# Optimization experiments

Measured on AMD Instinct MI355X. Metric: run time of the kernel, lower is better.

The kernel has to match this reference:

```python
import jax, jax.numpy as jnp
import numpy as np

N = 131072          # events
N_OBS = 64          # observables
HID = [512, 512, 512]          # trunk hidden widths
SUB_HID = [512, 256]           # per-pair subnetwork hidden widths
P = 3                          # number of pairings


def _glorot(key, shape):
    fan_in, fan_out = shape[-2], shape[-1]
    lim = np.sqrt(6.0 / (fan_in + fan_out)).astype(np.float32)
    return jax.random.uniform(key, shape, jnp.float32, -lim, lim)


def setup_inputs() -> dict:
    key = jax.random.key(0)
    ks = jax.random.split(key, 16)
    x = jax.random.normal(ks[0], (N, N_OBS), jnp.float32)
    y = jax.random.randint(ks[1], (N,), 0, 3)
    pairs = jnp.array([[0, 1], [0, 2], [1, 2]], dtype=jnp.int32)
    # trunk params
    W0 = _glorot(ks[2], (N_OBS, HID[0])); b0 = jnp.zeros((HID[0],), jnp.float32)
    W1 = _glorot(ks[3], (HID[0], HID[1])); b1 = jnp.zeros((HID[1],), jnp.float32)
    W2 = _glorot(ks[4], (HID[1], HID[2])); b2 = jnp.zeros((HID[2],), jnp.float32)
    # stacked per-pair subnetwork params (all P subnets share shapes)
    SW0 = _glorot(ks[5], (P, HID[2], SUB_HID[0])); Sb0 = jnp.zeros((P, SUB_HID[0]), jnp.float32)
    SW1 = _glorot(ks[6], (P, SUB_HID[0], SUB_HID[1])); Sb1 = jnp.zeros((P, SUB_HID[1]), jnp.float32)
    SW2 = _glorot(ks[7], (P, SUB_HID[1], 1)); Sb2 = jnp.zeros((P, 1), jnp.float32)
    return {"x": x, "y": y, "pairs": pairs,
            "W0": W0, "b0": b0, "W1": W1, "b1": b1, "W2": W2, "b2": b2,
            "SW0": SW0, "Sb0": Sb0, "SW1": SW1, "Sb1": Sb1, "SW2": SW2, "Sb2": Sb2}


def reference(x, y, pairs, W0, b0, W1, b1, W2, b2, SW0, Sb0, SW1, Sb1, SW2, Sb2):
    relu = jax.nn.relu
    # Trunk. Note: in the torch module with dropout_prob>0, the first Linear sits at
    # layer index 1, so the activation is applied to the raw input as well (eval-mode
    # dropout == identity). We reproduce that exactly.
    h = relu(x) @ W0 + b0
    h = relu(h) @ W1 + b1
    repr_ = relu(h) @ W2 + b2                      # [N, HID[-1]]

    # Per-pair membership masks (jit-safe stand-in for the variable-size gather):
    # mask[p, n] = True iff y[n] is one of the two labels of pairing p.
    mask = (y[None, :] == pairs[:, 0:1]) | (y[None, :] == pairs[:, 1:2])  # [P, N] bool

    # Per-pair RatioModel subnetworks, batched over the pair dim.
    # Same activation-before-every-Linear pattern as the trunk (dropout indices).
    hs = jnp.einsum('nd,pdh->pnh', relu(repr_), SW0) + Sb0[:, None, :]
    hs = jnp.einsum('pnh,phk->pnk', relu(hs), SW1) + Sb1[:, None, :]
    logit = jnp.einsum('pnk,pko->pno', relu(hs), SW2) + Sb2[:, None, :]  # [P, N, 1]
    s_hat = jnp.clip(jax.nn.sigmoid(logit[..., 0]), 1e-9, None)          # [P, N]
    r_hat = (1.0 - s_hat) / s_hat                                        # [P, N]

    maskf = mask.astype(s_hat.dtype)
    return repr_, r_hat * maskf, s_hat * maskf, mask
```

## Files before the change

### kernel.cpp

```cpp
#include <hip/hip_runtime.h>
#include <stdint.h>

#define NE 131072

typedef __attribute__((ext_vector_type(8))) short bf16x8;
typedef __attribute__((ext_vector_type(4))) float f32x4;

static __device__ __forceinline__ unsigned short f2bf(float f) {
  unsigned u = __float_as_uint(f);
  u += 0x7FFF + ((u >> 16) & 1);
  return (unsigned short)(u >> 16);
}
static __device__ __forceinline__ float bf2f(unsigned short h) {
  return __uint_as_float((unsigned)h << 16);
}
static __device__ __forceinline__ void gload_lds16(const void* g, void* l) {
  __builtin_amdgcn_global_load_lds(
      (const __attribute__((address_space(1))) unsigned*)g,
      (__attribute__((address_space(3))) unsigned*)l, 16, 0, 0);
}

__global__ void weight_prep(const float* __restrict__ W0, const float* __restrict__ W1,
                            const float* __restrict__ W2, const float* __restrict__ SW0,
                            const float* __restrict__ SW1, const float* __restrict__ SW2,
                            unsigned short* W0t, unsigned short* W1t,
                            unsigned short* W2t, unsigned short* SW0t,
                            unsigned short* SW1t, unsigned short* SW2b) {
  __shared__ float tile[32][33];
  const int u = blockIdx.y;
  const float* src; unsigned short* dst; int K, Nc;
  if (u == 0)      { src = W0;  dst = W0t;  K = 64;  Nc = 512; }
  else if (u == 1) { src = W1;  dst = W1t;  K = 512; Nc = 512; }
  else if (u == 2) { src = W2;  dst = W2t;  K = 512; Nc = 512; }
  else if (u < 6)  { int p = u - 3; src = SW0 + (long)p * 512 * 512; dst = SW0t + (long)p * 512 * 512; K = 512; Nc = 512; }
  else if (u < 9)  { int p = u - 6; src = SW1 + (long)p * 512 * 256; dst = SW1t + (long)p * 256 * 512; K = 512; Nc = 256; }
  else             { int p = u - 9; src = SW2 + (long)p * 256;       dst = SW2b + (long)p * 256;       K = 256; Nc = 1; }
  const int tkn = K >> 5;
  const int tk = blockIdx.x % tkn, tn = blockIdx.x / tkn;
  if (tn >= ((Nc + 31) >> 5)) return;
  const int k0 = tk * 32, n0 = tn * 32;
  const int tx = threadIdx.x & 31, ty = threadIdx.x >> 5;
  if (n0 + tx < Nc)
#pragma unroll
    for (int j = 0; j < 4; ++j)
      tile[ty * 4 + j][tx] = src[(long)(k0 + ty * 4 + j) * Nc + n0 + tx];
  __syncthreads();
#pragma unroll
  for (int j = 0; j < 4; ++j) {
    int n = n0 + ty * 4 + j;
    if (n < Nc) dst[(long)n * K + k0 + tx] = f2bf(tile[tx][ty * 4 + j]);
  }
}

__global__ void relu_cvt_x(const float4* __restrict__ x,
                           ushort4* __restrict__ xb) {
  int i = blockIdx.x * blockDim.x + threadIdx.x;
  float4 v = x[i];
  ushort4 o;
  o.x = f2bf(fmaxf(v.x, 0.f));
  o.y = f2bf(fmaxf(v.y, 0.f));
  o.z = f2bf(fmaxf(v.z, 0.f));
  o.w = f2bf(fmaxf(v.w, 0.f));
  xb[i] = o;
}

__global__ __launch_bounds__(512) void gemm2ph(
    const unsigned short* __restrict__ A, long aZ,
    const unsigned short* __restrict__ Bt, long bZ,
    const float* __restrict__ bias, long biasZ,
    float* __restrict__ outF,
    unsigned short* __restrict__ outA, long cZ,
    int K, int Nc,
    const unsigned short* __restrict__ w2, long w2Z,
    float* __restrict__ PB, long pbZ, int r0) {
  __shared__ unsigned short lds[2][1536 * 8];
  __shared__ float part[4][256];
  const int z = blockIdx.z;
  A += (long)z * aZ;
  Bt += (long)z * bZ;
  bias += (long)z * biasZ;
  if (outA) outA += (long)z * cZ;
  if (w2) { w2 += (long)z * w2Z; PB += (long)z * pbZ; }

  const int tid = threadIdx.x, wave = tid >> 6, lane = tid & 63;
  const int wm = wave >> 2, wn = wave & 3;
  const int lr = lane & 15, lh = lane >> 4;
  const long brow = (long)blockIdx.x * 256;
  const int bcol = blockIdx.y * 128;
  const int nk = K >> 5;
  const int axr = (lh ^ ((lr >> 1) & 3)) * 8;

  f32x4 acc[8][2];
#pragma unroll
  for (int m = 0; m < 8; ++m)
#pragma unroll
    for (int n = 0; n < 2; ++n) acc[m][n] = (f32x4){0.f, 0.f, 0.f, 0.f};

  auto STAGE = [&](int t) {
    unsigned short* dst = lds[t & 1];
    const int k0 = t << 5;
#pragma unroll
    for (int i = 0; i < 2; ++i) {
      const int cb = i * 512 + wave * 64;
      const int c = cb + lane;
      const int r = c >> 2;
      const int kc = (c & 3) ^ ((r >> 1) & 3);
      gload_lds16(A + (brow + r) * (long)K + k0 + kc * 8, &dst[cb * 8]);
    }
    {
      const int cb = wave * 64;
      const int c = cb + lane;
      const int r = c >> 2;
      const int kc = (c & 3) ^ ((r >> 1) & 3);
      gload_lds16(Bt + (long)(bcol + r) * K + k0 + kc * 8,
                  &dst[(1024 + cb) * 8]);
    }
  };

  STAGE(0);
  asm volatile("s_waitcnt vmcnt(0)" ::: "memory");
  __builtin_amdgcn_s_barrier();
  __builtin_amdgcn_sched_barrier(0);

  for (int t = 0; t < nk; ++t) {
    if (t + 1 < nk) STAGE(t + 1);
    const unsigned short* buf = lds[t & 1];
    bf16x8 a[8], b[2];
#pragma unroll
    for (int m = 0; m < 8; ++m)
      a[m] = *(const bf16x8*)&buf[(wm * 128 + m * 16 + lr) * 32 + axr];
#pragma unroll
    for (int n = 0; n < 2; ++n)
      b[n] = *(const bf16x8*)&buf[1024 * 8 + (wn * 32 + n * 16 + lr) * 32 + axr];
#pragma unroll
    for (int m = 0; m < 8; ++m)
#pragma unroll
      for (int n = 0; n < 2; ++n)
        acc[m][n] =
            __builtin_amdgcn_mfma_f32_16x16x32_bf16(a[m], b[n], acc[m][n], 0, 0, 0);
    asm volatile("s_waitcnt vmcnt(0)" ::: "memory");
    __builtin_amdgcn_s_barrier();
    __builtin_amdgcn_sched_barrier(0);
  }

  float bv[2];
#pragma unroll
  for (int n = 0; n < 2; ++n) bv[n] = bias[bcol + wn * 32 + n * 16 + lr];

  if (!w2) {
#pragma unroll
    for (int m = 0; m < 8; ++m) {
#pragma unroll
      for (int r = 0; r < 4; ++r) {
        long e = brow + wm * 128 + m * 16 + lh * 4 + r;
#pragma unroll
        for (int n = 0; n < 2; ++n) {
          int oc = bcol + wn * 32 + n * 16 + lr;
          float v = acc[m][n][r] + bv[n];
          if (outF) outF[e * Nc + oc] = v;
          if (outA) outA[e * Nc + oc] = f2bf(fmaxf(v, 0.f));
        }
      }
    }
  } else {
    float w2v[2];
#pragma unroll
    for (int n = 0; n < 2; ++n) w2v[n] = bf2f(w2[bcol + wn * 32 + n * 16 + lr]);
#pragma unroll
    for (int m = 0; m < 8; ++m) {
#pragma unroll
      for (int r = 0; r < 4; ++r) {
        float s = 0.f;
#pragma unroll
        for (int n = 0; n < 2; ++n)
          s += fmaxf(acc[m][n][r] + bv[n], 0.f) * w2v[n];
#pragma unroll
        for (int off = 1; off < 16; off <<= 1) s += __shfl_xor(s, off);
        if (lr == 0) part[wn][wm * 128 + m * 16 + lh * 4 + r] = s;
      }
    }
    __syncthreads();
    if (tid < 256)
      PB[(long)blockIdx.y * NE + r0 + brow + tid] =
          part[0][tid] + part[1][tid] + part[2][tid] + part[3][tid];
  }
}

__global__ void head_final(const float* __restrict__ PB,
                           const float* __restrict__ Sb2,
                           const int* __restrict__ y,
                           const int* __restrict__ pairs,
                           float* __restrict__ outR, float* __restrict__ outS,
                           float* __restrict__ outM) {
  const int n = blockIdx.x * 256 + threadIdx.x;
  const int p = blockIdx.y;
  float logit = PB[(long)p * 2 * NE + n] + PB[(long)(p * 2 + 1) * NE + n] +
                Sb2[p];
  float s = 1.f / (1.f + expf(-logit));
  s = fmaxf(s, 1e-9f);
  float r = (1.f - s) / s;
  int yv = y[n];
  float mf = (yv == pairs[p * 2] || yv == pairs[p * 2 + 1]) ? 1.f : 0.f;
  outR[(long)p * NE + n] = r * mf;
  outS[(long)p * NE + n] = s * mf;
  outM[(long)p * NE + n] = mf;
}

extern "C" void kernel_launch(void* const* d_in, const int* in_sizes, int n_in,
                              void* d_out, int out_size, void* d_ws, size_t ws_size,
                              hipStream_t stream) {
  const float* x   = (const float*)d_in[0];
  const int*   y   = (const int*)d_in[1];
  const int*   prs = (const int*)d_in[2];
  const float* W0  = (const float*)d_in[3];
  const float* b0  = (const float*)d_in[4];
  const float* W1  = (const float*)d_in[5];
  const float* b1  = (const float*)d_in[6];
  const float* W2  = (const float*)d_in[7];
  const float* b2  = (const float*)d_in[8];
  const float* SW0 = (const float*)d_in[9];
  const float* Sb0 = (const float*)d_in[10];
  const float* SW1 = (const float*)d_in[11];
  const float* Sb1 = (const float*)d_in[12];
  const float* SW2 = (const float*)d_in[13];
  const float* Sb2 = (const float*)d_in[14];

  uint8_t* ws = (uint8_t*)d_ws;
  size_t off = 0;
  auto take = [&](size_t bytes) -> void* {
    void* ptr = ws + off;
    off = (off + bytes + 255) & ~(size_t)255;
    return ptr;
  };
  unsigned short* W0t  = (unsigned short*)take((size_t)64 * 512 * 2);
  unsigned short* W1t  = (unsigned short*)take((size_t)512 * 512 * 2);
  unsigned short* W2t  = (unsigned short*)take((size_t)512 * 512 * 2);
  unsigned short* SW0t = (unsigned short*)take((size_t)3 * 512 * 512 * 2);
  unsigned short* SW1t = (unsigned short*)take((size_t)3 * 256 * 512 * 2);
  unsigned short* SW2b = (unsigned short*)take((size_t)3 * 256 * 2);
  unsigned short* Xb   = (unsigned short*)take((size_t)NE * 64 * 2);
  float*          PB   = (float*)take((size_t)6 * NE * 4);
  const size_t fixed = off;

  long chunk = 32768;
  while (chunk > 8192 && fixed + (size_t)6 * chunk * 1024 + 4096 > ws_size)
    chunk >>= 1;

  unsigned short* T0   = (unsigned short*)take((size_t)chunk * 512 * 2);
  unsigned short* T1   = (unsigned short*)take((size_t)chunk * 512 * 2);
  unsigned short* bufR = (unsigned short*)take((size_t)chunk * 512 * 2);
  unsigned short* H3   = (unsigned short*)take((size_t)3 * chunk * 512 * 2);

  float* out   = (float*)d_out;
  float* outRe = out;
  float* outR  = out + (size_t)NE * 512;
  float* outS  = outR + (size_t)3 * NE;
  float* outM  = outS + (size_t)3 * NE;

  weight_prep<<<dim3(256, 12), 256, 0, stream>>>(W0, W1, W2, SW0, SW1, SW2,
                                                 W0t, W1t, W2t, SW0t, SW1t, SW2b);
  relu_cvt_x<<<dim3(NE * 64 / 4 / 256), 256, 0, stream>>>((const float4*)x,
                                                          (ushort4*)Xb);

  for (long r0 = 0; r0 < NE; r0 += chunk) {
    gemm2ph<<<dim3(chunk / 256, 4, 1), 512, 0, stream>>>(
        Xb + r0 * 64, 0, W0t, 0, b0, 0, nullptr, T0, 0, 64, 512,
        nullptr, 0, nullptr, 0, 0);
    gemm2ph<<<dim3(chunk / 256, 4, 1), 512, 0, stream>>>(
        T0, 0, W1t, 0, b1, 0, nullptr, T1, 0, 512, 512,
        nullptr, 0, nullptr, 0, 0);
    gemm2ph<<<dim3(chunk / 256, 4, 1), 512, 0, stream>>>(
        T1, 0, W2t, 0, b2, 0, outRe + r0 * 512, bufR, 0, 512, 512,
        nullptr, 0, nullptr, 0, 0);
    gemm2ph<<<dim3(chunk / 256, 4, 3), 512, 0, stream>>>(
        bufR, 0, SW0t, (long)512 * 512, Sb0, 512, nullptr,
        H3, (long)chunk * 512, 512, 512,
        nullptr, 0, nullptr, 0, 0);
    gemm2ph<<<dim3(chunk / 256, 2, 3), 512, 0, stream>>>(
        H3, (long)chunk * 512, SW1t, (long)256 * 512, Sb1, 256, nullptr,
        nullptr, 0, 512, 256,
        SW2b, 256, PB, (long)2 * NE, (int)r0);
  }
  head_final<<<dim3(NE / 256, 3), 256, 0, stream>>>(PB, Sb2, y, prs,
                                                    outR, outS, outM);
}
```

Measured before the change: 735.8 us.

## Triple-buffer GEMM LDS pipeline with BK=64 and interleaved load rounds

Replaces the double-buffered BK=32 GEMM mainloop with a three-stage LDS ring using BK=64 tiles and an 8-slot XOR swizzle. Global-to-LDS loads for the next two k-steps are split into rounds interleaved between two half-tiles of MFMA work, with partial vmcnt waits and s_setprio around MFMA blocks. The aim is to hide global-load latency and remove a full barrier per k-step. In exchange it uses more LDS (144KB), which may limit occupancy, and the reduction scratch now aliases the LDS buffer, so an extra sync is needed.

```diff
diff --git a/kernel.cpp b/kernel.cpp
--- a/kernel.cpp
+++ b/kernel.cpp
@@ -64,7 +64,7 @@
   xb[i] = o;
 }
 
-__global__ __launch_bounds__(512) void gemm2ph(
+__global__ __launch_bounds__(512) void gemm3r(
     const unsigned short* __restrict__ A, long aZ,
     const unsigned short* __restrict__ Bt, long bZ,
     const float* __restrict__ bias, long biasZ,
@@ -73,8 +73,7 @@
     int K, int Nc,
     const unsigned short* __restrict__ w2, long w2Z,
     float* __restrict__ PB, long pbZ, int r0) {
-  __shared__ unsigned short lds[2][1536 * 8];
-  __shared__ float part[4][256];
+  __shared__ unsigned short lds[3 * 24576];
   const int z = blockIdx.z;
   A += (long)z * aZ;
   Bt += (long)z * bZ;
@@ -87,8 +86,7 @@
   const int lr = lane & 15, lh = lane >> 4;
   const long brow = (long)blockIdx.x * 256;
   const int bcol = blockIdx.y * 128;
-  const int nk = K >> 5;
-  const int axr = (lh ^ ((lr >> 1) & 3)) * 8;
+  const int nk = K >> 6;
 
   f32x4 acc[8][2];
 #pragma unroll
@@ -96,51 +94,87 @@
 #pragma unroll
     for (int n = 0; n < 2; ++n) acc[m][n] = (f32x4){0.f, 0.f, 0.f, 0.f};
 
-  auto STAGE = [&](int t) {
-    unsigned short* dst = lds[t & 1];
-    const int k0 = t << 5;
-#pragma unroll
-    for (int i = 0; i < 2; ++i) {
-      const int cb = i * 512 + wave * 64;
+  auto ROUND = [&](int t, int rnd) {
+    if ((unsigned)t >= (unsigned)nk) return;
+    unsigned short* buf = &lds[(t % 3) * 24576];
+    const int k0 = t << 6;
+    if (rnd < 4) {
+      const int cb = rnd * 512 + wave * 64;
       const int c = cb + lane;
-      const int r = c >> 2;
-      const int kc = (c & 3) ^ ((r >> 1) & 3);
-      gload_lds16(A + (brow + r) * (long)K + k0 + kc * 8, &dst[cb * 8]);
-    }
-    {
-      const int cb = wave * 64;
+      const int row = c >> 3, sl = c & 7;
+      const int kc = sl ^ (row & 7);
+      gload_lds16(A + (brow + row) * (long)K + k0 + kc * 8, &buf[cb * 8]);
+    } else {
+      const int cb = (rnd - 4) * 512 + wave * 64;
       const int c = cb + lane;
-      const int r = c >> 2;
-      const int kc = (c & 3) ^ ((r >> 1) & 3);
-      gload_lds16(Bt + (long)(bcol + r) * K + k0 + kc * 8,
-                  &dst[(1024 + cb) * 8]);
+      const int row = c >> 3, sl = c & 7;
+      const int kc = sl ^ (row & 7);
+      gload_lds16(Bt + (long)(bcol + row) * K + k0 + kc * 8,
+                  &buf[16384 + cb * 8]);
     }
   };
 
-  STAGE(0);
-  asm volatile("s_waitcnt vmcnt(0)" ::: "memory");
-  __builtin_amdgcn_s_barrier();
-  __builtin_amdgcn_sched_barrier(0);
+#pragma unroll
+  for (int r = 0; r < 6; ++r) ROUND(0, r);
+  ROUND(1, 0); ROUND(1, 1);
+
+  const int sl0 = (0 * 4 + lh) ^ (lr & 7);
+  const int sl1 = (1 * 4 + lh) ^ (lr & 7);
 
   for (int t = 0; t < nk; ++t) {
-    if (t + 1 < nk) STAGE(t + 1);
-    const unsigned short* buf = lds[t & 1];
-    bf16x8 a[8], b[2];
-#pragma unroll
-    for (int m = 0; m < 8; ++m)
-      a[m] = *(const bf16x8*)&buf[(wm * 128 + m * 16 + lr) * 32 + axr];
-#pragma unroll
-    for (int n = 0; n < 2; ++n)
-      b[n] = *(const bf16x8*)&buf[1024 * 8 + (wn * 32 + n * 16 + lr) * 32 + axr];
-#pragma unroll
-    for (int m = 0; m < 8; ++m)
+    if (t < nk - 1)
+      asm volatile("s_waitcnt vmcnt(2)" ::: "memory");
+    else
+      asm volatile("s_waitcnt vmcnt(0)" ::: "memory");
+    __builtin_amdgcn_s_barrier();
+    const unsigned short* buf = &lds[(t % 3) * 24576];
+    const char* bufc = (const char*)buf;
+
+    bf16x8 a[4][2], b[2][2];
+#pragma unroll
+    for (int m = 0; m < 4; ++m) {
+      const int row = wm * 128 + m * 16 + lr;
+      a[m][0] = *(const bf16x8*)(bufc + row * 128 + sl0 * 16);
+      a[m][1] = *(const bf16x8*)(bufc + row * 128 + sl1 * 16);
+    }
+#pragma unroll
+    for (int n = 0; n < 2; ++n) {
+      const int row = wn * 32 + n * 16 + lr;
+      b[n][0] = *(const bf16x8*)(bufc + 32768 + row * 128 + sl0 * 16);
+      b[n][1] = *(const bf16x8*)(bufc + 32768 + row * 128 + sl1 * 16);
+    }
+    ROUND(t + 1, 2); ROUND(t + 1, 3); ROUND(t + 1, 4); ROUND(t + 1, 5);
+    asm volatile("s_waitcnt lgkmcnt(0)" ::: "memory");
+    __builtin_amdgcn_sched_barrier(0);
+    __builtin_amdgcn_s_setprio(1);
+#pragma unroll
+    for (int m = 0; m < 4; ++m)
 #pragma unroll
       for (int n = 0; n < 2; ++n)
-        acc[m][n] =
-            __builtin_amdgcn_mfma_f32_16x16x32_bf16(a[m], b[n], acc[m][n], 0, 0, 0);
-    asm volatile("s_waitcnt vmcnt(0)" ::: "memory");
-    __builtin_amdgcn_s_barrier();
+#pragma unroll
+        for (int kk = 0; kk < 2; ++kk)
+          acc[m][n] = __builtin_amdgcn_mfma_f32_16x16x32_bf16(
+              a[m][kk], b[n][kk], acc[m][n], 0, 0, 0);
+    __builtin_amdgcn_s_setprio(0);
+#pragma unroll
+    for (int m = 0; m < 4; ++m) {
+      const int row = wm * 128 + (m + 4) * 16 + lr;
+      a[m][0] = *(const bf16x8*)(bufc + row * 128 + sl0 * 16);
+      a[m][1] = *(const bf16x8*)(bufc + row * 128 + sl1 * 16);
+    }
+    ROUND(t + 2, 0); ROUND(t + 2, 1);
+    asm volatile("s_waitcnt lgkmcnt(0)" ::: "memory");
     __builtin_amdgcn_sched_barrier(0);
+    __builtin_amdgcn_s_setprio(1);
+#pragma unroll
+    for (int m = 0; m < 4; ++m)
+#pragma unroll
+      for (int n = 0; n < 2; ++n)
+#pragma unroll
+        for (int kk = 0; kk < 2; ++kk)
+          acc[m + 4][n] = __builtin_amdgcn_mfma_f32_16x16x32_bf16(
+              a[m][kk], b[n][kk], acc[m + 4][n], 0, 0, 0);
+    __builtin_amdgcn_s_setprio(0);
   }
 
   float bv[2];
@@ -163,6 +197,8 @@
       }
     }
   } else {
+    float* part = (float*)lds;
+    __syncthreads();
     float w2v[2];
 #pragma unroll
     for (int n = 0; n < 2; ++n) w2v[n] = bf2f(w2[bcol + wn * 32 + n * 16 + lr]);
@@ -176,13 +212,13 @@
           s += fmaxf(acc[m][n][r] + bv[n], 0.f) * w2v[n];
 #pragma unroll
         for (int off = 1; off < 16; off <<= 1) s += __shfl_xor(s, off);
-        if (lr == 0) part[wn][wm * 128 + m * 16 + lh * 4 + r] = s;
+        if (lr == 0) part[wn * 256 + wm * 128 + m * 16 + lh * 4 + r] = s;
       }
     }
     __syncthreads();
     if (tid < 256)
       PB[(long)blockIdx.y * NE + r0 + brow + tid] =
-          part[0][tid] + part[1][tid] + part[2][tid] + part[3][tid];
+          part[tid] + part[256 + tid] + part[512 + tid] + part[768 + tid];
   }
 }
 
@@ -263,20 +299,20 @@
                                                           (ushort4*)Xb);
 
   for (long r0 = 0; r0 < NE; r0 += chunk) {
-    gemm2ph<<<dim3(chunk / 256, 4, 1), 512, 0, stream>>>(
+    gemm3r<<<dim3(chunk / 256, 4, 1), 512, 0, stream>>>(
         Xb + r0 * 64, 0, W0t, 0, b0, 0, nullptr, T0, 0, 64, 512,
         nullptr, 0, nullptr, 0, 0);
-    gemm2ph<<<dim3(chunk / 256, 4, 1), 512, 0, stream>>>(
+    gemm3r<<<dim3(chunk / 256, 4, 1), 512, 0, stream>>>(
         T0, 0, W1t, 0, b1, 0, nullptr, T1, 0, 512, 512,
         nullptr, 0, nullptr, 0, 0);
-    gemm2ph<<<dim3(chunk / 256, 4, 1), 512, 0, stream>>>(
+    gemm3r<<<dim3(chunk / 256, 4, 1), 512, 0, stream>>>(
         T1, 0, W2t, 0, b2, 0, outRe + r0 * 512, bufR, 0, 512, 512,
         nullptr, 0, nullptr, 0, 0);
-    gemm2ph<<<dim3(chunk / 256, 4, 3), 512, 0, stream>>>(
+    gemm3r<<<dim3(chunk / 256, 4, 3), 512, 0, stream>>>(
         bufR, 0, SW0t, (long)512 * 512, Sb0, 512, nullptr,
         H3, (long)chunk * 512, 512, 512,
         nullptr, 0, nullptr, 0, 0);
-    gemm2ph<<<dim3(chunk / 256, 2, 3), 512, 0, stream>>>(
+    gemm3r<<<dim3(chunk / 256, 2, 3), 512, 0, stream>>>(
         H3, (long)chunk * 512, SW1t, (long)256 * 512, Sb1, 256, nullptr,
         nullptr, 0, 512, 256,
         SW2b, 256, PB, (long)2 * NE, (int)r0);
```

Measured after the change: 788.6 us. 1.07x slower.
